# Optimization experiments

Hardware: AMD Instinct MI355X
Metric: run time of the kernel (lower is better)

The kernel has to match this reference:

```python
import jax, jax.numpy as jnp
import numpy as np

T = 1024          # tokens (batch*seq, vLLM flattened layout)
D = 2048          # hidden_size
H = 16            # attention heads
HD = D // H       # head_dim = 128
E = 16            # num routed experts
K = 2             # top_k
IM = 1408         # moe_intermediate_size
IS = 5632         # shared_expert_intermediate_size
EPS = 1e-6
THETA = 10000.0


def setup_inputs() -> dict:
    key = jax.random.key(0)
    ks = jax.random.split(key, 14)
    s = 0.02  # weight scale
    n = jax.random.normal
    return {
        "positions": jnp.arange(T, dtype=jnp.int32),
        "hidden_states": n(ks[0], (T, D), jnp.float32),
        "ln1_w": 1.0 + s * n(ks[1], (D,), jnp.float32),
        "ln2_w": 1.0 + s * n(ks[2], (D,), jnp.float32),
        "qkv_w": s * n(ks[3], (D, 3 * H * HD), jnp.float32),
        "qkv_b": s * n(ks[4], (3 * H * HD,), jnp.float32),
        "o_w": s * n(ks[5], (H * HD, D), jnp.float32),
        "router_w": s * n(ks[6], (D, E), jnp.float32),
        "w_gate": s * n(ks[7], (E, D, IM), jnp.float32),
        "w_up": s * n(ks[8], (E, D, IM), jnp.float32),
        "w_down": s * n(ks[9], (E, IM, D), jnp.float32),
        "sh_gate_up": s * n(ks[10], (D, 2 * IS), jnp.float32),
        "sh_down": s * n(ks[11], (IS, D), jnp.float32),
        "sh_expert_gate": s * n(ks[12], (D, 1), jnp.float32),
    }


def _rmsnorm(x, w):
    var = jnp.mean(x * x, axis=-1, keepdims=True)
    return x * jax.lax.rsqrt(var + EPS) * w


def _rope(x, positions):
    # neox-style rotary: x [T, H, HD]
    half = HD // 2
    inv_freq = 1.0 / (THETA ** (jnp.arange(0, half, dtype=jnp.float32) / half * 1.0))
    inv_freq = 1.0 / (THETA ** (jnp.arange(0, HD, 2, dtype=jnp.float32) / HD))
    ang = positions.astype(jnp.float32)[:, None] * inv_freq  # [T, HD/2]
    cos = jnp.cos(ang)[:, None, :]
    sin = jnp.sin(ang)[:, None, :]
    x1, x2 = x[..., :half], x[..., half:]
    return jnp.concatenate([x1 * cos - x2 * sin, x2 * cos + x1 * sin], axis=-1)


def reference(positions, hidden_states, ln1_w, ln2_w, qkv_w, qkv_b, o_w,
              router_w, w_gate, w_up, w_down, sh_gate_up, sh_down,
              sh_expert_gate):
    # --- input RMSNorm (residual=None path) ---
    residual = hidden_states
    x = _rmsnorm(hidden_states, ln1_w)

    # --- self-attention: QKV + RoPE + causal SDPA + o_proj ---
    qkv = x @ qkv_w + qkv_b
    q, k, v = jnp.split(qkv, [H * HD, 2 * H * HD], axis=-1)
    q = _rope(q.reshape(T, H, HD), positions)
    k = _rope(k.reshape(T, H, HD), positions)
    v = v.reshape(T, H, HD)
    scale = HD ** -0.5
    scores = jnp.einsum('thd,shd->hts', q, k) * scale  # [H, T, T]
    causal = jnp.tril(jnp.ones((T, T), dtype=bool))
    scores = jnp.where(causal[None], scores, jnp.finfo(scores.dtype).min)
    attn = jax.nn.softmax(scores, axis=-1)
    ctx = jnp.einsum('hts,shd->thd', attn, v).reshape(T, H * HD)
    attn_out = ctx @ o_w

    # --- fused add + post-attention RMSNorm ---
    residual = residual + attn_out
    x = _rmsnorm(residual, ln2_w)

    # --- sparse MoE: router -> softmax -> top-k (renormalized) -> experts ---
    logits = x @ router_w                                    # [T, E]
    probs = jax.nn.softmax(logits.astype(jnp.float32), axis=-1)
    topv, topi = jax.lax.top_k(probs, K)                     # [T, K]
    topv = topv / jnp.sum(topv, axis=-1, keepdims=True)      # norm_topk_prob
    w = jnp.zeros((T, E), dtype=x.dtype).at[
        jnp.arange(T)[:, None], topi].set(topv.astype(x.dtype))
    g = jax.nn.silu(jnp.einsum('td,edi->tei', x, w_gate)) * \
        jnp.einsum('td,edi->tei', x, w_up)                   # [T, E, IM]
    moe_out = jnp.einsum('tei,eid,te->td', g, w_down, w)

    # --- shared expert with sigmoid gate ---
    gu = x @ sh_gate_up
    g2, u2 = jnp.split(gu, 2, axis=-1)
    shared = (jax.nn.silu(g2) * u2) @ sh_down
    shared = jax.nn.sigmoid(x @ sh_expert_gate) * shared

    hidden_states = moe_out + shared
    return hidden_states, residual
```

## Files before the change

kernel.cpp:

```cpp
#include <hip/hip_runtime.h>

constexpr int T_  = 1024;
constexpr int D_  = 2048;
constexpr int H_  = 16;
constexpr int HD_ = 128;
constexpr int E_  = 16;
constexpr int IM_ = 1408;
constexpr int IS_ = 5632;

typedef __attribute__((ext_vector_type(8))) short bf16x8;
typedef __attribute__((ext_vector_type(4))) short short4v;
typedef __attribute__((ext_vector_type(4))) float f32x4;

__device__ __forceinline__ short f2bf(float f){
  unsigned u = __builtin_bit_cast(unsigned, f);
  u += 0x7fffu + ((u >> 16) & 1u);
  return (short)(u >> 16);
}
__device__ __forceinline__ float bf2f(short s){
  unsigned u = ((unsigned)(unsigned short)s) << 16;
  return __builtin_bit_cast(float, u);
}
__device__ __forceinline__ unsigned cvtpk(float lo, float hi){
  unsigned r;
  asm("v_cvt_pk_bf16_f32 %0, %1, %2" : "=v"(r) : "v"(lo), "v"(hi));
  return r;
}
__device__ __forceinline__ float pk_lo(unsigned h){
  return __builtin_bit_cast(float, h << 16);
}
__device__ __forceinline__ float pk_hi(unsigned h){
  return __builtin_bit_cast(float, h & 0xffff0000u);
}
__device__ __forceinline__ f32x4 mfma16(bf16x8 a, bf16x8 b, f32x4 c){
  return __builtin_amdgcn_mfma_f32_16x16x32_bf16(a, b, c, 0, 0, 0);
}
__device__ __forceinline__ void split3(float f, short& h, short& m, short& l){
  h = f2bf(f); float r = f - bf2f(h);
  m = f2bf(r); l = f2bf(r - bf2f(m));
}
__device__ __forceinline__ void split2(float f, short& h, short& m){
  h = f2bf(f); m = f2bf(f - bf2f(h));
}
__device__ __forceinline__ uint4 mk4(unsigned a, unsigned b, unsigned c, unsigned d){
  uint4 r; r.x=a; r.y=b; r.z=c; r.w=d; return r;
}

__global__ __launch_bounds__(256) void sctab_kernel(
    const int* __restrict__ pos, float* __restrict__ cst, float* __restrict__ snt)
{
  int idx = blockIdx.x * 256 + threadIdx.x;
  if (idx >= T_ * 64) return;
  int t = idx >> 6, i = idx & 63;
  float invf = (float)pow(10000.0, -(double)i / 64.0);
  float ang  = (float)pos[t] * invf;
  double s, c;
  sincos((double)ang, &s, &c);
  cst[idx] = (float)c; snt[idx] = (float)s;
}

__global__ __launch_bounds__(256) void rms_kernel(
    const float* __restrict__ x, const float* __restrict__ w,
    short* __restrict__ o0, short* __restrict__ o1, short* __restrict__ o2,
    short* __restrict__ ob, float* __restrict__ of)
{
  int t = blockIdx.x, tid = threadIdx.x;
  const float* xr = x + (size_t)t * D_;
  float4 va = ((const float4*)xr)[tid*2];
  float4 vb = ((const float4*)xr)[tid*2+1];
  float ss = va.x*va.x + va.y*va.y + va.z*va.z + va.w*va.w
           + vb.x*vb.x + vb.y*vb.y + vb.z*vb.z + vb.w*vb.w;
  for (int o = 32; o; o >>= 1) ss += __shfl_xor(ss, o, 64);
  __shared__ float red[4];
  int lane = tid & 63, wid = tid >> 6;
  if (lane == 0) red[wid] = ss;
  __syncthreads();
  ss = red[0] + red[1] + red[2] + red[3];
  float rs = 1.0f / sqrtf(ss * (1.0f/D_) + 1e-6f);
  float4 wa = ((const float4*)w)[tid*2];
  float4 wb = ((const float4*)w)[tid*2+1];
  float xv[8] = {va.x,va.y,va.z,va.w, vb.x,vb.y,vb.z,vb.w};
  float wv[8] = {wa.x,wa.y,wa.z,wa.w, wb.x,wb.y,wb.z,wb.w};
  size_t base = (size_t)t * D_ + tid*8;
  #pragma unroll
  for (int p = 0; p < 4; ++p){
    float f0 = xv[2*p]   * rs * wv[2*p];
    float f1 = xv[2*p+1] * rs * wv[2*p+1];
    if (o0){
      unsigned h = cvtpk(f0, f1);
      float r0 = f0 - pk_lo(h), r1 = f1 - pk_hi(h);
      unsigned m = cvtpk(r0, r1);
      unsigned l = cvtpk(r0 - pk_lo(m), r1 - pk_hi(m));
      *(unsigned*)&o0[base + 2*p] = h;
      *(unsigned*)&o1[base + 2*p] = m;
      *(unsigned*)&o2[base + 2*p] = l;
    }
    if (ob) *(unsigned*)&ob[base + 2*p] = cvtpk(f0, f1);
    if (of){ of[base + 2*p] = f0; of[base + 2*p + 1] = f1; }
  }
}

__global__ __launch_bounds__(256) void prepk_kernel(
    const float* __restrict__ qkv, const float* __restrict__ cst,
    const float* __restrict__ snt, short* __restrict__ Kp0, short* __restrict__ Kp1)
{
  int idx = blockIdx.x * 256 + threadIdx.x;
  int c = idx & 7, t = (idx >> 3) & (T_-1), h = idx >> 13;
  int d0 = c * 8;
  const float* kp = qkv + (size_t)t * (3*D_) + D_ + h*HD_;
  const float* cp = cst + t*64 + d0;
  const float* sp = snt + t*64 + d0;
  unsigned lh[4], ll[4], hh[4], hl[4];
  #pragma unroll
  for (int p = 0; p < 4; ++p){
    float xl0 = kp[d0+2*p],    xh0 = kp[d0+64+2*p];
    float xl1 = kp[d0+2*p+1],  xh1 = kp[d0+64+2*p+1];
    float cv0 = cp[2*p], sv0 = sp[2*p], cv1 = cp[2*p+1], sv1 = sp[2*p+1];
    float rl0 = xl0*cv0 - xh0*sv0, rh0 = xh0*cv0 + xl0*sv0;
    float rl1 = xl1*cv1 - xh1*sv1, rh1 = xh1*cv1 + xl1*sv1;
    unsigned a = cvtpk(rl0, rl1);
    ll[p] = cvtpk(rl0 - pk_lo(a), rl1 - pk_hi(a)); lh[p] = a;
    unsigned b = cvtpk(rh0, rh1);
    hl[p] = cvtpk(rh0 - pk_lo(b), rh1 - pk_hi(b)); hh[p] = b;
  }
  size_t ob = ((size_t)h*T_ + t) * HD_;
  *(uint4*)(Kp0 + ob + d0)      = mk4(lh[0],lh[1],lh[2],lh[3]);
  *(uint4*)(Kp0 + ob + 64 + d0) = mk4(hh[0],hh[1],hh[2],hh[3]);
  *(uint4*)(Kp1 + ob + d0)      = mk4(ll[0],ll[1],ll[2],ll[3]);
  *(uint4*)(Kp1 + ob + 64 + d0) = mk4(hl[0],hl[1],hl[2],hl[3]);
}

__global__ __launch_bounds__(256) void prepv_kernel(
    const float* __restrict__ qkv, short* __restrict__ Vp0, short* __restrict__ Vp1)
{
  __shared__ short Vl[2][128][72];
  int t0 = blockIdx.x * 64, h = blockIdx.y, tid = threadIdx.x;
  int r = tid >> 2, cq = (tid & 3) * 32;
  const float* src = qkv + (size_t)(t0+r) * (3*D_) + 2*D_ + h*HD_ + cq;
  #pragma unroll
  for (int jj = 0; jj < 8; ++jj){
    float4 v = *(const float4*)(src + jj*4);
    float vv[4] = {v.x, v.y, v.z, v.w};
    #pragma unroll
    for (int u = 0; u < 4; ++u){
      int d = cq + jj*4 + u;
      short a, b; split2(vv[u], a, b);
      Vl[0][d][r] = a; Vl[1][d][r] = b;
    }
  }
  __syncthreads();
  int d = tid >> 1, tc = (tid & 1) * 32;
  short* dst0 = Vp0 + ((size_t)h*HD_ + d) * T_ + t0 + tc;
  short* dst1 = Vp1 + ((size_t)h*HD_ + d) * T_ + t0 + tc;
  #pragma unroll
  for (int q = 0; q < 4; ++q){
    *(uint4*)(dst0 + q*8) = *(const uint4*)&Vl[0][d][tc + q*8];
    *(uint4*)(dst1 + q*8) = *(const uint4*)&Vl[1][d][tc + q*8];
  }
}

__global__ __launch_bounds__(256) void prepw_kernel(
    const float* __restrict__ w, short* __restrict__ P0, short* __restrict__ P1)
{
  __shared__ short L0[64][72], L1[64][72];
  int k0 = blockIdx.x * 64, n0 = blockIdx.y * 64;
  int tid = threadIdx.x;
  int r = tid >> 2, cq = (tid & 3) * 16;
  const float* src = w + (size_t)(k0 + r) * D_ + n0 + cq;
  #pragma unroll
  for (int q = 0; q < 4; ++q){
    float4 f = *(const float4*)(src + q*4);
    float fv[4] = {f.x, f.y, f.z, f.w};
    #pragma unroll
    for (int u = 0; u < 4; ++u){
      int n = cq + q*4 + u;
      short a, b; split2(fv[u], a, b);
      L0[n][r] = a; L1[n][r] = b;
    }
  }
  __syncthreads();
  int n = tid >> 2, kq = (tid & 3) * 16;
  short* d0 = P0 + (size_t)(n0 + n) * D_ + k0 + kq;
  short* d1 = P1 + (size_t)(n0 + n) * D_ + k0 + kq;
  *(uint4*)(d0)     = *(const uint4*)&L0[n][kq];
  *(uint4*)(d0 + 8) = *(const uint4*)&L0[n][kq + 8];
  *(uint4*)(d1)     = *(const uint4*)&L1[n][kq];
  *(uint4*)(d1 + 8) = *(const uint4*)&L1[n][kq + 8];
}

__global__ __launch_bounds__(128) void attn_kernel(
    const float* __restrict__ qkv,
    const float* __restrict__ cst, const float* __restrict__ snt,
    const short* __restrict__ Kp0, const short* __restrict__ Kp1,
    const short* __restrict__ Vp0, const short* __restrict__ Vp1,
    short* __restrict__ c0p, short* __restrict__ c1p, short* __restrict__ c2p)
{
  __shared__ __attribute__((aligned(16))) short Ks[2][2][32][128];
  __shared__ __attribute__((aligned(16))) short Vs[2][2][128][40];
  __shared__ __attribute__((aligned(16))) short Ps[3][2][16][40];

  const float SCALE = 0.08838834764831845f;
  const int QW = 3*D_;
  int h = blockIdx.x;
  int ys = blockIdx.y;
  int qt = (ys < 16) ? (ys*2) : ((31-ys)*2 + 1);
  int q0 = qt * 32;
  int tid = threadIdx.x, lane = tid & 63, wq = tid >> 6;
  int lr = lane & 15, kq8 = (lane >> 4) * 8, r4 = (lane >> 4) * 4;

  bf16x8 qfh[4], qfm[4], qfl[4];
  { int qrow = q0 + wq*16 + lr;
    const float* qp = qkv + (size_t)qrow * QW + h*HD_;
    const float* cp = cst + qrow*64;
    const float* sp = snt + qrow*64;
    float x[4][8], cs[2][8], sn[2][8], rot[4][8];
    for (int ks = 0; ks < 4; ++ks)
      for (int j = 0; j < 8; ++j) x[ks][j] = qp[ks*32 + kq8 + j];
    for (int hf = 0; hf < 2; ++hf)
      for (int j = 0; j < 8; ++j){
        cs[hf][j] = cp[hf*32 + kq8 + j];
        sn[hf][j] = sp[hf*32 + kq8 + j];
      }
    for (int j = 0; j < 8; ++j){
      rot[0][j] = x[0][j]*cs[0][j] - x[2][j]*sn[0][j];
      rot[1][j] = x[1][j]*cs[1][j] - x[3][j]*sn[1][j];
      rot[2][j] = x[2][j]*cs[0][j] + x[0][j]*sn[0][j];
      rot[3][j] = x[3][j]*cs[1][j] + x[1][j]*sn[1][j];
    }
    for (int ks = 0; ks < 4; ++ks)
      for (int j = 0; j < 8; ++j){
        short a, b, c; split3(rot[ks][j], a, b, c);
        qfh[ks][j] = a; qfm[ks][j] = b; qfl[ks][j] = c;
      }
  }

  f32x4 acc[8];
  for (int i = 0; i < 8; ++i) acc[i] = f32x4{0.f,0.f,0.f,0.f};
  float mrun[4] = {-1e30f,-1e30f,-1e30f,-1e30f};
  float lrun[4] = {0.f,0.f,0.f,0.f};

  int krow = tid >> 2, kc = (tid & 3) * 32;
  const short* kb0 = Kp0 + ((size_t)h*T_ + krow) * HD_ + kc;
  const short* kb1 = Kp1 + ((size_t)h*T_ + krow) * HD_ + kc;
  const short* vb0 = Vp0 + ((size_t)h*HD_ + tid) * T_;
  const short* vb1 = Vp1 + ((size_t)h*HD_ + tid) * T_;
  int xr = (krow & 7) * 8;

  uint4 kr0[4], kr1[4], vr0[4], vr1[4];
  auto LOAD = [&](int it){
    size_t ko = (size_t)it * 32 * HD_;
    const uint4* p0 = (const uint4*)(kb0 + ko);
    const uint4* p1 = (const uint4*)(kb1 + ko);
    #pragma unroll
    for (int g = 0; g < 4; ++g){ kr0[g] = p0[g]; kr1[g] = p1[g]; }
    const uint4* q0p = (const uint4*)(vb0 + it*32);
    const uint4* q1p = (const uint4*)(vb1 + it*32);
    #pragma unroll
    for (int g = 0; g < 4; ++g){ vr0[g] = q0p[g]; vr1[g] = q1p[g]; }
  };
  auto STORE = [&](int buf){
    #pragma unroll
    for (int g = 0; g < 4; ++g){
      int col = (kc + 8*g) ^ xr;
      *(uint4*)&Ks[buf][0][krow][col] = kr0[g];
      *(uint4*)&Ks[buf][1][krow][col] = kr1[g];
    }
    #pragma unroll
    for (int g = 0; g < 4; ++g){
      *(uint4*)&Vs[buf][0][tid][g*8] = vr0[g];
      *(uint4*)&Vs[buf][1][tid][g*8] = vr1[g];
    }
  };

  int nt = qt + 1;
  LOAD(0); STORE(0);
  if (nt > 1) LOAD(1);
  asm volatile("s_waitcnt lgkmcnt(0)" ::: "memory");
  __builtin_amdgcn_s_barrier();

  int cur = 0;
  for (int it = 0; it < nt; ++it){
    if (it + 1 < nt){
      STORE(cur ^ 1);
      if (it + 2 < nt) LOAD(it + 2);
    }
    int kv0 = it * 32;
    int xl = (lr & 7) * 8;
    f32x4 s0 = f32x4{0.f,0.f,0.f,0.f}, s1 = f32x4{0.f,0.f,0.f,0.f};
    #pragma unroll
    for (int ks = 0; ks < 4; ++ks){
      int col = (ks*32 + kq8) ^ xl;
      bf16x8 b0h = *(const bf16x8*)&Ks[cur][0][lr][col];
      bf16x8 b0m = *(const bf16x8*)&Ks[cur][1][lr][col];
      bf16x8 b1h = *(const bf16x8*)&Ks[cur][0][16+lr][col];
      bf16x8 b1m = *(const bf16x8*)&Ks[cur][1][16+lr][col];
      s0 = mfma16(qfh[ks], b0h, s0); s0 = mfma16(qfh[ks], b0m, s0);
      s0 = mfma16(qfm[ks], b0h, s0); s0 = mfma16(qfm[ks], b0m, s0);
      s0 = mfma16(qfl[ks], b0h, s0);
      s1 = mfma16(qfh[ks], b1h, s1); s1 = mfma16(qfh[ks], b1m, s1);
      s1 = mfma16(qfm[ks], b1h, s1); s1 = mfma16(qfm[ks], b1m, s1);
      s1 = mfma16(qfl[ks], b1h, s1);
    }
    float pm[2][4]; float alpha[4];
    for (int r = 0; r < 4; ++r){
      int qr = q0 + wq*16 + r4 + r;
      float x0 = s0[r]*SCALE, x1 = s1[r]*SCALE;
      if (kv0 + lr > qr)      x0 = -1e30f;
      if (kv0 + 16 + lr > qr) x1 = -1e30f;
      float mt_ = fmaxf(x0, x1);
      mt_ = fmaxf(mt_, __shfl_xor(mt_, 1, 64));
      mt_ = fmaxf(mt_, __shfl_xor(mt_, 2, 64));
      mt_ = fmaxf(mt_, __shfl_xor(mt_, 4, 64));
      mt_ = fmaxf(mt_, __shfl_xor(mt_, 8, 64));
      float mn = fmaxf(mrun[r], mt_);
      float p0 = __expf(x0 - mn), p1 = __expf(x1 - mn);
      pm[0][r] = p0; pm[1][r] = p1;
      float ls = p0 + p1;
      ls += __shfl_xor(ls, 1, 64); ls += __shfl_xor(ls, 2, 64);
      ls += __shfl_xor(ls, 4, 64); ls += __shfl_xor(ls, 8, 64);
      alpha[r] = __expf(mrun[r] - mn);
      lrun[r] = lrun[r]*alpha[r] + ls;
      mrun[r] = mn;
    }
    for (int dt = 0; dt < 8; ++dt){
      f32x4 a = acc[dt];
      a[0]*=alpha[0]; a[1]*=alpha[1]; a[2]*=alpha[2]; a[3]*=alpha[3];
      acc[dt] = a;
    }
    for (int nn = 0; nn < 2; ++nn)
      for (int r = 0; r < 4; ++r){
        short a, b, c; split3(pm[nn][r], a, b, c);
        Ps[0][wq][r4+r][nn*16+lr] = a;
        Ps[1][wq][r4+r][nn*16+lr] = b;
        Ps[2][wq][r4+r][nn*16+lr] = c;
      }
    bf16x8 pah = *(const bf16x8*)&Ps[0][wq][lr][kq8];
    bf16x8 pam = *(const bf16x8*)&Ps[1][wq][lr][kq8];
    bf16x8 pal = *(const bf16x8*)&Ps[2][wq][lr][kq8];
    #pragma unroll
    for (int dt = 0; dt < 8; ++dt){
      bf16x8 vbh = *(const bf16x8*)&Vs[cur][0][dt*16+lr][kq8];
      bf16x8 vbm = *(const bf16x8*)&Vs[cur][1][dt*16+lr][kq8];
      acc[dt] = mfma16(pah, vbh, acc[dt]);
      acc[dt] = mfma16(pah, vbm, acc[dt]);
      acc[dt] = mfma16(pam, vbh, acc[dt]);
      acc[dt] = mfma16(pam, vbm, acc[dt]);
      acc[dt] = mfma16(pal, vbh, acc[dt]);
    }
    asm volatile("s_waitcnt lgkmcnt(0)" ::: "memory");
    __builtin_amdgcn_s_barrier();
    cur ^= 1;
  }
  for (int dt = 0; dt < 8; ++dt)
    for (int r = 0; r < 4; ++r){
      int qr = q0 + wq*16 + r4 + r;
      float o = acc[dt][r] / lrun[r];
      size_t ix = (size_t)qr * D_ + h*HD_ + dt*16 + lr;
      short a, b, c; split3(o, a, b, c);
      c0p[ix] = a; c1p[ix] = b; c2p[ix] = c;
    }
}

enum { M_QKV = 0, M_OPROJ = 1 };

template<int MODE>
__global__ __launch_bounds__(256) void gemm3_kernel(
    const short* __restrict__ A0, const short* __restrict__ A1, const short* __restrict__ A2,
    const float* __restrict__ Bw,
    const short* __restrict__ Bp0, const short* __restrict__ Bp1,
    const float* __restrict__ bias, const float* __restrict__ addsrc,
    float* __restrict__ outF,
    int K, int lda, int ldb, int ldo)
{
  __shared__ __attribute__((aligned(16))) short As[2][3][64][40];
  __shared__ __attribute__((aligned(16))) short Bs[2][2][64][40];

  int m0 = blockIdx.y * 64, n0 = blockIdx.x * 64;
  int tid = threadIdx.x, lane = tid & 63, wid = tid >> 6;
  int wm = wid >> 1, wn = wid & 1;
  int lr = lane & 15, kq8 = (lane >> 4) * 8;

  f32x4 acc[2][2];
  for (int i = 0; i < 2; ++i)
    for (int j = 0; j < 2; ++j) acc[i][j] = f32x4{0.f,0.f,0.f,0.f};

  int arow = tid >> 2, ac = (tid & 3) * 8;
  const short* aP0 = A0 + (size_t)(m0 + arow) * lda + ac;
  const short* aP1 = A1 + (size_t)(m0 + arow) * lda + ac;
  const short* aP2 = A2 + (size_t)(m0 + arow) * lda + ac;
  int bn = tid & 63, bk0 = (tid >> 6) * 8;
  const float* bP  = Bw  ? (Bw + n0 + bn) : nullptr;
  const short* bq0 = Bp0 ? (Bp0 + (size_t)(n0 + bn) * K) : nullptr;
  const short* bq1 = Bp1 ? (Bp1 + (size_t)(n0 + bn) * K) : nullptr;

  uint4 ar0, ar1, ar2;
  float br[8];
  uint4 pb0, pb1;

  auto LOAD = [&](int kt){
    ar0 = *(const uint4*)(aP0 + kt*32);
    ar1 = *(const uint4*)(aP1 + kt*32);
    ar2 = *(const uint4*)(aP2 + kt*32);
    if constexpr (MODE == M_QKV){
      const float* p = bP + (size_t)(kt*32 + bk0) * ldb;
      #pragma unroll
      for (int j = 0; j < 8; ++j) br[j] = p[(size_t)j * ldb];
    } else {
      pb0 = *(const uint4*)(bq0 + kt*32 + bk0);
      pb1 = *(const uint4*)(bq1 + kt*32 + bk0);
    }
  };
  auto STORE = [&](int buf){
    *(uint4*)&As[buf][0][arow][ac] = ar0;
    *(uint4*)&As[buf][1][arow][ac] = ar1;
    *(uint4*)&As[buf][2][arow][ac] = ar2;
    if constexpr (MODE == M_QKV){
      unsigned hh[4], mm[4];
      #pragma unroll
      for (int p = 0; p < 4; ++p){
        float f0 = br[2*p], f1 = br[2*p+1];
        unsigned h = cvtpk(f0, f1);
        mm[p] = cvtpk(f0 - pk_lo(h), f1 - pk_hi(h));
        hh[p] = h;
      }
      *(uint4*)&Bs[buf][0][bn][bk0] = mk4(hh[0],hh[1],hh[2],hh[3]);
      *(uint4*)&Bs[buf][1][bn][bk0] = mk4(mm[0],mm[1],mm[2],mm[3]);
    } else {
      *(uint4*)&Bs[buf][0][bn][bk0] = pb0;
      *(uint4*)&Bs[buf][1][bn][bk0] = pb1;
    }
  };

  int NK = K / 32;
  LOAD(0); STORE(0);
  if (NK > 1) LOAD(1);
  asm volatile("s_waitcnt lgkmcnt(0)" ::: "memory");
  __builtin_amdgcn_s_barrier();

  int cur = 0;
  for (int kt = 0; kt < NK; ++kt){
    if (kt + 1 < NK){
      STORE(cur ^ 1);
      if (kt + 2 < NK) LOAD(kt + 2);
    }
    bf16x8 aH[2], aM[2], aL[2];
    #pragma unroll
    for (int mt = 0; mt < 2; ++mt){
      aH[mt] = *(const bf16x8*)&As[cur][0][wm*32 + mt*16 + lr][kq8];
      aM[mt] = *(const bf16x8*)&As[cur][1][wm*32 + mt*16 + lr][kq8];
      aL[mt] = *(const bf16x8*)&As[cur][2][wm*32 + mt*16 + lr][kq8];
    }
    #pragma unroll
    for (int nt = 0; nt < 2; ++nt){
      bf16x8 bH = *(const bf16x8*)&Bs[cur][0][wn*32 + nt*16 + lr][kq8];
      bf16x8 bM = *(const bf16x8*)&Bs[cur][1][wn*32 + nt*16 + lr][kq8];
      #pragma unroll
      for (int mt = 0; mt < 2; ++mt){
        f32x4 a = acc[mt][nt];
        a = mfma16(aH[mt], bH, a);
        a = mfma16(aH[mt], bM, a);
        a = mfma16(aM[mt], bH, a);
        a = mfma16(aM[mt], bM, a);
        a = mfma16(aL[mt], bH, a);
        acc[mt][nt] = a;
      }
    }
    asm volatile("s_waitcnt lgkmcnt(0)" ::: "memory");
    __builtin_amdgcn_s_barrier();
    cur ^= 1;
  }

  for (int mt = 0; mt < 2; ++mt)
    for (int nt = 0; nt < 2; ++nt)
      for (int r = 0; r < 4; ++r){
        int mrow = m0 + wm*32 + mt*16 + (lane >> 4)*4 + r;
        int col  = n0 + wn*32 + nt*16 + lr;
        float v = acc[mt][nt][r];
        if constexpr (MODE == M_QKV){
          outF[(size_t)mrow * ldo + col] = v + bias[col];
        } else {
          outF[(size_t)mrow * ldo + col] = v + addsrc[(size_t)mrow * ldo + col];
        }
      }
}

__global__ __launch_bounds__(256) void gu_kernel(
    const short* __restrict__ x2b,
    const float* __restrict__ w_gate, const float* __restrict__ w_up,
    const float* __restrict__ sh_gu,
    short* __restrict__ gbuf, short* __restrict__ sbuf,
    const int* __restrict__ perm, const int* __restrict__ offE,
    const int* __restrict__ cntE)
{
  __shared__ __attribute__((aligned(16))) short As[2][128][40];
  __shared__ __attribute__((aligned(16))) short Bs[2][2][64][40];

  int z = blockIdx.z;
  bool SH = (z == E_);
  int N    = SH ? IS_ : IM_;
  int n0 = blockIdx.x * 64;
  if (n0 >= N) return;
  int mcnt  = SH ? T_ : cntE[z];
  int mbase = SH ? 0  : offE[z];
  int m0 = blockIdx.y * 128;
  if (m0 >= mcnt) return;
  int ldb = SH ? 2*IS_ : IM_;
  int ldo = SH ? IS_   : IM_;
  const float* Bg = SH ? sh_gu        : (w_gate + (size_t)z * D_ * IM_);
  const float* Bu = SH ? (sh_gu + IS_) : (w_up  + (size_t)z * D_ * IM_);
  short* outB = SH ? sbuf : gbuf;

  int tid = threadIdx.x, lane = tid & 63, wid = tid >> 6;
  int wm = wid >> 1, wn = wid & 1;
  int lr = lane & 15, kq8 = (lane >> 4) * 8;

  f32x4 acc0[4][2], acc1[4][2];
  #pragma unroll
  for (int i = 0; i < 4; ++i)
    for (int j = 0; j < 2; ++j){
      acc0[i][j] = f32x4{0.f,0.f,0.f,0.f};
      acc1[i][j] = f32x4{0.f,0.f,0.f,0.f};
    }

  int arow = tid >> 1, acol = (tid & 1) * 16;
  int aRowIdx;
  { int mr = m0 + arow;
    int mc = (mr < mcnt) ? mr : 0;
    aRowIdx = SH ? mc : perm[mbase + mc];
  }
  const short* aP = x2b + (size_t)aRowIdx * D_;

  int bn_ = tid & 63, bkq = (tid >> 6) * 8;
  const float* bP0 = Bg + n0 + bn_;
  const float* bP1 = Bu + n0 + bn_;

  uint4 arA, arB;
  float br0[8], br1[8];

  auto LOAD = [&](int kt){
    const uint4* s = (const uint4*)(aP + kt*32 + acol);
    arA = s[0]; arB = s[1];
    const float* p0 = bP0 + (size_t)(kt*32 + bkq) * ldb;
    const float* p1 = bP1 + (size_t)(kt*32 + bkq) * ldb;
    #pragma unroll
    for (int j = 0; j < 8; ++j){ br0[j] = p0[(size_t)j * ldb]; br1[j] = p1[(size_t)j * ldb]; }
  };
  auto STORE = [&](int buf){
    *(uint4*)&As[buf][arow][acol]   = arA;
    *(uint4*)&As[buf][arow][acol+8] = arB;
    unsigned v0[4], v1[4];
    #pragma unroll
    for (int p = 0; p < 4; ++p){
      v0[p] = cvtpk(br0[2*p], br0[2*p+1]);
      v1[p] = cvtpk(br1[2*p], br1[2*p+1]);
    }
    *(uint4*)&Bs[buf][0][bn_][bkq] = mk4(v0[0],v0[1],v0[2],v0[3]);
    *(uint4*)&Bs[buf][1][bn_][bkq] = mk4(v1[0],v1[1],v1[2],v1[3]);
  };

  constexpr int NK = D_ / 32;
  LOAD(0); STORE(0);
  LOAD(1);
  asm volatile("s_waitcnt lgkmcnt(0)" ::: "memory");
  __builtin_amdgcn_s_barrier();

  int cur = 0;
  for (int kt = 0; kt < NK; ++kt){
    if (kt + 1 < NK){
      STORE(cur ^ 1);
      if (kt + 2 < NK) LOAD(kt + 2);
    }
    bf16x8 a[4];
    #pragma unroll
    for (int mt = 0; mt < 4; ++mt)
      a[mt] = *(const bf16x8*)&As[cur][wm*64 + mt*16 + lr][kq8];
    #pragma unroll
    for (int nt = 0; nt < 2; ++nt){
      int nrow = wn*32 + nt*16 + lr;
      bf16x8 b0 = *(const bf16x8*)&Bs[cur][0][nrow][kq8];
      bf16x8 b1 = *(const bf16x8*)&Bs[cur][1][nrow][kq8];
      #pragma unroll
      for (int mt = 0; mt < 4; ++mt){
        acc0[mt][nt] = mfma16(a[mt], b0, acc0[mt][nt]);
        acc1[mt][nt] = mfma16(a[mt], b1, acc1[mt][nt]);
      }
    }
    asm volatile("s_waitcnt lgkmcnt(0)" ::: "memory");
    __builtin_amdgcn_s_barrier();
    cur ^= 1;
  }

  for (int mt = 0; mt < 4; ++mt)
    for (int nt = 0; nt < 2; ++nt)
      for (int r = 0; r < 4; ++r){
        int mrow = m0 + wm*64 + mt*16 + (lane >> 4)*4 + r;
        if (mrow >= mcnt) continue;
        int col = n0 + wn*32 + nt*16 + lr;
        float v = acc0[mt][nt][r];
        float u = acc1[mt][nt][r];
        float sv = v / (1.f + __expf(-v)) * u;
        outB[(size_t)(mbase + mrow) * ldo + col] = f2bf(sv);
      }
}

__global__ __launch_bounds__(256) void dn_kernel(
    const short* __restrict__ gbuf, const short* __restrict__ sbuf,
    const float* __restrict__ w_down, const float* __restrict__ sh_down,
    float* __restrict__ outF,
    const int* __restrict__ perm, const int* __restrict__ offE,
    const int* __restrict__ cntE, const float* __restrict__ wgt,
    const float* __restrict__ sig)
{
  __shared__ __attribute__((aligned(16))) short As[2][128][40];
  __shared__ __attribute__((aligned(16))) short Bs[2][64][40];

  int z = blockIdx.z;
  bool SH = (z == E_);
  int K = SH ? IS_ : IM_;
  int mcnt  = SH ? T_ : cntE[z];
  int mbase = SH ? 0  : offE[z];
  int m0 = blockIdx.y * 128;
  if (m0 >= mcnt) return;
  int n0 = blockIdx.x * 64;
  const float* Bq = SH ? sh_down : (w_down + (size_t)z * IM_ * D_);
  const short* Ab = SH ? sbuf : gbuf;

  int tid = threadIdx.x, lane = tid & 63, wid = tid >> 6;
  int wm = wid >> 1, wn = wid & 1;
  int lr = lane & 15, kq8 = (lane >> 4) * 8;

  f32x4 acc0[4][2];
  #pragma unroll
  for (int i = 0; i < 4; ++i)
    for (int j = 0; j < 2; ++j) acc0[i][j] = f32x4{0.f,0.f,0.f,0.f};

  int arow = tid >> 1, acol = (tid & 1) * 16;
  int mr = m0 + arow;
  int mc = (mr < mcnt) ? mr : 0;
  const short* aP = Ab + (size_t)(SH ? mc : (mbase + mc)) * K;

  int bn_ = tid & 63, bkq = (tid >> 6) * 8;
  const float* bP0 = Bq + n0 + bn_;

  uint4 arA, arB;
  float br0[8];

  auto LOAD = [&](int kt){
    const uint4* s = (const uint4*)(aP + kt*32 + acol);
    arA = s[0]; arB = s[1];
    const float* p0 = bP0 + (size_t)(kt*32 + bkq) * D_;
    #pragma unroll
    for (int j = 0; j < 8; ++j) br0[j] = p0[(size_t)j * D_];
  };
  auto STORE = [&](int buf){
    *(uint4*)&As[buf][arow][acol]   = arA;
    *(uint4*)&As[buf][arow][acol+8] = arB;
    unsigned v0[4];
    #pragma unroll
    for (int p = 0; p < 4; ++p) v0[p] = cvtpk(br0[2*p], br0[2*p+1]);
    *(uint4*)&Bs[buf][bn_][bkq] = mk4(v0[0],v0[1],v0[2],v0[3]);
  };

  int NK = K / 32;
  LOAD(0); STORE(0);
  LOAD(1);
  asm volatile("s_waitcnt lgkmcnt(0)" ::: "memory");
  __builtin_amdgcn_s_barrier();

  int cur = 0;
  for (int kt = 0; kt < NK; ++kt){
    if (kt + 1 < NK){
      STORE(cur ^ 1);
      if (kt + 2 < NK) LOAD(kt + 2);
    }
    bf16x8 a[4];
    #pragma unroll
    for (int mt = 0; mt < 4; ++mt)
      a[mt] = *(const bf16x8*)&As[cur][wm*64 + mt*16 + lr][kq8];
    #pragma unroll
    for (int nt = 0; nt < 2; ++nt){
      bf16x8 b0 = *(const bf16x8*)&Bs[cur][wn*32 + nt*16 + lr][kq8];
      #pragma unroll
      for (int mt = 0; mt < 4; ++mt)
        acc0[mt][nt] = mfma16(a[mt], b0, acc0[mt][nt]);
    }
    asm volatile("s_waitcnt lgkmcnt(0)" ::: "memory");
    __builtin_amdgcn_s_barrier();
    cur ^= 1;
  }

  for (int mt = 0; mt < 4; ++mt)
    for (int nt = 0; nt < 2; ++nt)
      for (int r = 0; r < 4; ++r){
        int mrow = m0 + wm*64 + mt*16 + (lane >> 4)*4 + r;
        if (mrow >= mcnt) continue;
        int col = n0 + wn*32 + nt*16 + lr;
        float v = acc0[mt][nt][r];
        if (SH){
          atomicAdd(&outF[(size_t)mrow * D_ + col], sig[mrow] * v);
        } else {
          int tk = perm[mbase + mrow];
          atomicAdd(&outF[(size_t)tk * D_ + col], v * wgt[mbase + mrow]);
        }
      }
}

__global__ __launch_bounds__(256) void router_kernel(
    const float* __restrict__ x2f, const float* __restrict__ rw,
    const float* __restrict__ seg, int* __restrict__ te, float* __restrict__ tw,
    float* __restrict__ sig, int* __restrict__ cnt)
{
  int t = blockIdx.x, tid = threadIdx.x, lane = tid & 63, w = tid >> 6;
  const float* xr = x2f + (size_t)t * D_;
  float a0 = 0.f, a1 = 0.f, a2 = 0.f, a3 = 0.f, ag = 0.f;
  for (int j = 0; j < 32; ++j){
    int d = lane + 64*j;
    float xv = xr[d];
    const float* rp = rw + (size_t)d * E_ + w*4;
    a0 += xv * rp[0]; a1 += xv * rp[1]; a2 += xv * rp[2]; a3 += xv * rp[3];
    ag += xv * seg[d];
  }
  for (int o = 32; o; o >>= 1){
    a0 += __shfl_xor(a0, o, 64); a1 += __shfl_xor(a1, o, 64);
    a2 += __shfl_xor(a2, o, 64); a3 += __shfl_xor(a3, o, 64);
    ag += __shfl_xor(ag, o, 64);
  }
  __shared__ float lg[16];
  __shared__ float sgv;
  if (lane == 0){
    lg[w*4+0] = a0; lg[w*4+1] = a1; lg[w*4+2] = a2; lg[w*4+3] = a3;
    if (w == 0) sgv = ag;
  }
  __syncthreads();
  if (tid == 0){
    int e0 = 0; float v0 = lg[0];
    for (int ee = 1; ee < 16; ++ee) if (lg[ee] > v0){ v0 = lg[ee]; e0 = ee; }
    int e1 = -1; float v1 = -3e38f;
    for (int ee = 0; ee < 16; ++ee){
      if (ee == e0) continue;
      if (lg[ee] > v1){ v1 = lg[ee]; e1 = ee; }
    }
    float w0 = 1.f / (1.f + expf(v1 - v0));
    te[2*t] = e0; te[2*t+1] = e1;
    tw[2*t] = w0; tw[2*t+1] = 1.f - w0;
    atomicAdd(&cnt[e0], 1); atomicAdd(&cnt[e1], 1);
    sig[t] = 1.f / (1.f + expf(-sgv));
  }
}

__global__ void prefix_kernel(const int* __restrict__ cnt, int* __restrict__ offE,
                              int* __restrict__ cursor)
{
  if (threadIdx.x == 0){
    int s = 0;
    for (int e = 0; e < 16; ++e){ offE[e] = s; s += cnt[e]; }
  }
  if (threadIdx.x < 16) cursor[threadIdx.x] = 0;
}

__global__ __launch_bounds__(256) void scatter_kernel(
    const int* __restrict__ te, const float* __restrict__ tw,
    const int* __restrict__ offE, int* __restrict__ cursor,
    int* __restrict__ perm, float* __restrict__ wgt)
{
  int t = blockIdx.x * 256 + threadIdx.x;
  if (t >= T_) return;
  for (int i = 0; i < 2; ++i){
    int e = te[2*t + i];
    int pos = offE[e] + atomicAdd(&cursor[e], 1);
    perm[pos] = t; wgt[pos] = tw[2*t + i];
  }
}

extern "C" void kernel_launch(void* const* d_in, const int* in_sizes, int n_in,
                              void* d_out, int out_size, void* d_ws, size_t ws_size,
                              hipStream_t stream)
{
  const int*   positions = (const int*)  d_in[0];
  const float* hidden    = (const float*)d_in[1];
  const float* ln1       = (const float*)d_in[2];
  const float* ln2       = (const float*)d_in[3];
  const float* qkv_w     = (const float*)d_in[4];
  const float* qkv_b     = (const float*)d_in[5];
  const float* o_w       = (const float*)d_in[6];
  const float* router_w  = (const float*)d_in[7];
  const float* w_gate    = (const float*)d_in[8];
  const float* w_up      = (const float*)d_in[9];
  const float* w_down    = (const float*)d_in[10];
  const float* sh_gu     = (const float*)d_in[11];
  const float* sh_down   = (const float*)d_in[12];
  const float* sh_eg     = (const float*)d_in[13];

  float* out_hidden = (float*)d_out;
  float* out_resid  = (float*)d_out + (size_t)T_ * D_;

  char* wp = (char*)d_ws;
  auto alloc = [&](size_t b){ char* p = wp; wp += (b + 255) & ~(size_t)255; return p; };

  float* qkv  = (float*)alloc((size_t)T_ * 3*D_ * 4);
  short* x1h  = (short*)alloc((size_t)T_ * D_ * 2);
  short* x1m  = (short*)alloc((size_t)T_ * D_ * 2);
  short* x1l  = (short*)alloc((size_t)T_ * D_ * 2);
  short* Kp0  = (short*)alloc((size_t)T_ * D_ * 2);
  short* Kp1  = (short*)alloc((size_t)T_ * D_ * 2);
  short* Vp0  = (short*)alloc((size_t)T_ * D_ * 2);
  short* Vp1  = (short*)alloc((size_t)T_ * D_ * 2);
  float* cst  = (float*)alloc((size_t)T_ * 64 * 4);
  float* snt  = (float*)alloc((size_t)T_ * 64 * 4);
  int*   te   = (int*)  alloc(2*T_*4);
  float* tw   = (float*)alloc(2*T_*4);
  float* sig  = (float*)alloc(T_*4);
  int*   cnt    = (int*)alloc(256);
  int*   offE   = (int*)alloc(256);
  int*   cursor = (int*)alloc(256);
  int*   perm = (int*)  alloc(2*T_*4);
  float* wgt  = (float*)alloc(2*T_*4);

  short* ctxh = x1h;
  short* ctxm = x1m;
  short* ctxl = x1l;
  float* x2f  = qkv;
  short* sbuf = (short*)((char*)qkv + (size_t)8388608);
  short* gbuf = (short*)x1h;
  short* x2b  = (short*)((char*)x1h + (size_t)5767168);
  short* Wo0  = Kp0;
  short* Wo1  = Vp0;

  hipMemsetAsync(cnt, 0, 64, stream);
  hipMemsetAsync(out_hidden, 0, (size_t)T_ * D_ * 4, stream);

  sctab_kernel<<<(T_*64)/256, 256, 0, stream>>>(positions, cst, snt);

  rms_kernel<<<T_, 256, 0, stream>>>(hidden, ln1, x1h, x1m, x1l, nullptr, nullptr);

  gemm3_kernel<M_QKV><<<dim3(96, 16), 256, 0, stream>>>(
      x1h, x1m, x1l, qkv_w, nullptr, nullptr, qkv_b, nullptr, qkv,
      D_, D_, 3*D_, 3*D_);

  prepk_kernel<<<(T_*H_*8)/256, 256, 0, stream>>>(qkv, cst, snt, Kp0, Kp1);
  prepv_kernel<<<dim3(16, 16), 256, 0, stream>>>(qkv, Vp0, Vp1);

  attn_kernel<<<dim3(16, 32), 128, 0, stream>>>(
      qkv, cst, snt, Kp0, Kp1, Vp0, Vp1, ctxh, ctxm, ctxl);

  prepw_kernel<<<dim3(32, 32), 256, 0, stream>>>(o_w, Wo0, Wo1);

  gemm3_kernel<M_OPROJ><<<dim3(32, 16), 256, 0, stream>>>(
      ctxh, ctxm, ctxl, nullptr, Wo0, Wo1, nullptr, hidden, out_resid,
      D_, D_, D_, D_);

  rms_kernel<<<T_, 256, 0, stream>>>(out_resid, ln2, nullptr, nullptr, nullptr, x2b, x2f);

  router_kernel<<<T_, 256, 0, stream>>>(x2f, router_w, sh_eg, te, tw, sig, cnt);
  prefix_kernel<<<1, 64, 0, stream>>>(cnt, offE, cursor);
  scatter_kernel<<<4, 256, 0, stream>>>(te, tw, offE, cursor, perm, wgt);

  gu_kernel<<<dim3(88, 8, 17), 256, 0, stream>>>(
      x2b, w_gate, w_up, sh_gu, gbuf, sbuf, perm, offE, cnt);

  dn_kernel<<<dim3(32, 8, 17), 256, 0, stream>>>(
      gbuf, sbuf, w_down, sh_down, out_hidden, perm, offE, cnt, wgt, sig);

  (void)in_sizes; (void)n_in; (void)out_size; (void)ws_size;
}
```

Measured before the change: 876.3 us.

## Deepen GEMM global-load prefetch to two tiles ahead with dual register sets

The three GEMM kernels (gemm3, gate/up, down) now keep two register staging sets and unroll the k-loop by two. Global loads for tile kt+2 or kt+3 are issued while earlier tiles are stored to LDS and computed, so each load has more time in flight before it is consumed. The trade-off is higher register pressure, which could lower occupancy. Odd-NK handling relies on guards, and the gate/up and down loops assume an even NK.

```diff
diff --git a/kernel.cpp b/kernel.cpp
--- a/kernel.cpp
+++ b/kernel.cpp
@@ -45,6 +45,8 @@
 __device__ __forceinline__ uint4 mk4(unsigned a, unsigned b, unsigned c, unsigned d){
   uint4 r; r.x=a; r.y=b; r.z=c; r.w=d; return r;
 }
+#define LGKM0_BAR() do{ asm volatile("s_waitcnt lgkmcnt(0)" ::: "memory"); \
+                        __builtin_amdgcn_s_barrier(); }while(0)
 
 __global__ __launch_bounds__(256) void sctab_kernel(
     const int* __restrict__ pos, float* __restrict__ cst, float* __restrict__ snt)
@@ -275,8 +277,7 @@
   int nt = qt + 1;
   LOAD(0); STORE(0);
   if (nt > 1) LOAD(1);
-  asm volatile("s_waitcnt lgkmcnt(0)" ::: "memory");
-  __builtin_amdgcn_s_barrier();
+  LGKM0_BAR();
 
   int cur = 0;
   for (int it = 0; it < nt; ++it){
@@ -347,8 +348,7 @@
       acc[dt] = mfma16(pam, vbm, acc[dt]);
       acc[dt] = mfma16(pal, vbh, acc[dt]);
     }
-    asm volatile("s_waitcnt lgkmcnt(0)" ::: "memory");
-    __builtin_amdgcn_s_barrier();
+    LGKM0_BAR();
     cur ^= 1;
   }
   for (int dt = 0; dt < 8; ++dt)
@@ -393,56 +393,75 @@
   const short* bq0 = Bp0 ? (Bp0 + (size_t)(n0 + bn) * K) : nullptr;
   const short* bq1 = Bp1 ? (Bp1 + (size_t)(n0 + bn) * K) : nullptr;
 
-  uint4 ar0, ar1, ar2;
-  float br[8];
-  uint4 pb0, pb1;
-
-  auto LOAD = [&](int kt){
-    ar0 = *(const uint4*)(aP0 + kt*32);
-    ar1 = *(const uint4*)(aP1 + kt*32);
-    ar2 = *(const uint4*)(aP2 + kt*32);
+  uint4 ar0_0, ar1_0, ar2_0, ar0_1, ar1_1, ar2_1;
+  float br_0[8], br_1[8];
+  uint4 pb0_0, pb1_0, pb0_1, pb1_1;
+
+  auto LOAD0 = [&](int kt){
+    ar0_0 = *(const uint4*)(aP0 + kt*32);
+    ar1_0 = *(const uint4*)(aP1 + kt*32);
+    ar2_0 = *(const uint4*)(aP2 + kt*32);
     if constexpr (MODE == M_QKV){
       const float* p = bP + (size_t)(kt*32 + bk0) * ldb;
       #pragma unroll
-      for (int j = 0; j < 8; ++j) br[j] = p[(size_t)j * ldb];
+      for (int j = 0; j < 8; ++j) br_0[j] = p[(size_t)j * ldb];
     } else {
-      pb0 = *(const uint4*)(bq0 + kt*32 + bk0);
-      pb1 = *(const uint4*)(bq1 + kt*32 + bk0);
-    }
-  };
-  auto STORE = [&](int buf){
-    *(uint4*)&As[buf][0][arow][ac] = ar0;
-    *(uint4*)&As[buf][1][arow][ac] = ar1;
-    *(uint4*)&As[buf][2][arow][ac] = ar2;
+      pb0_0 = *(const uint4*)(bq0 + kt*32 + bk0);
+      pb1_0 = *(const uint4*)(bq1 + kt*32 + bk0);
+    }
+  };
+  auto LOAD1 = [&](int kt){
+    ar0_1 = *(const uint4*)(aP0 + kt*32);
+    ar1_1 = *(const uint4*)(aP1 + kt*32);
+    ar2_1 = *(const uint4*)(aP2 + kt*32);
+    if constexpr (MODE == M_QKV){
+      const float* p = bP + (size_t)(kt*32 + bk0) * ldb;
+      #pragma unroll
+      for (int j = 0; j < 8; ++j) br_1[j] = p[(size_t)j * ldb];
+    } else {
+      pb0_1 = *(const uint4*)(bq0 + kt*32 + bk0);
+      pb1_1 = *(const uint4*)(bq1 + kt*32 + bk0);
+    }
+  };
+  auto STORE0 = [&](int buf){
+    *(uint4*)&As[buf][0][arow][ac] = ar0_0;
+    *(uint4*)&As[buf][1][arow][ac] = ar1_0;
+    *(uint4*)&As[buf][2][arow][ac] = ar2_0;
     if constexpr (MODE == M_QKV){
       unsigned hh[4], mm[4];
       #pragma unroll
       for (int p = 0; p < 4; ++p){
-        float f0 = br[2*p], f1 = br[2*p+1];
-        unsigned h = cvtpk(f0, f1);
-        mm[p] = cvtpk(f0 - pk_lo(h), f1 - pk_hi(h));
+        unsigned h = cvtpk(br_0[2*p], br_0[2*p+1]);
+        mm[p] = cvtpk(br_0[2*p] - pk_lo(h), br_0[2*p+1] - pk_hi(h));
         hh[p] = h;
       }
       *(uint4*)&Bs[buf][0][bn][bk0] = mk4(hh[0],hh[1],hh[2],hh[3]);
       *(uint4*)&Bs[buf][1][bn][bk0] = mk4(mm[0],mm[1],mm[2],mm[3]);
     } else {
-      *(uint4*)&Bs[buf][0][bn][bk0] = pb0;
-      *(uint4*)&Bs[buf][1][bn][bk0] = pb1;
-    }
-  };
-
-  int NK = K / 32;
-  LOAD(0); STORE(0);
-  if (NK > 1) LOAD(1);
-  asm volatile("s_waitcnt lgkmcnt(0)" ::: "memory");
-  __builtin_amdgcn_s_barrier();
-
-  int cur = 0;
-  for (int kt = 0; kt < NK; ++kt){
-    if (kt + 1 < NK){
-      STORE(cur ^ 1);
-      if (kt + 2 < NK) LOAD(kt + 2);
-    }
+      *(uint4*)&Bs[buf][0][bn][bk0] = pb0_0;
+      *(uint4*)&Bs[buf][1][bn][bk0] = pb1_0;
+    }
+  };
+  auto STORE1 = [&](int buf){
+    *(uint4*)&As[buf][0][arow][ac] = ar0_1;
+    *(uint4*)&As[buf][1][arow][ac] = ar1_1;
+    *(uint4*)&As[buf][2][arow][ac] = ar2_1;
+    if constexpr (MODE == M_QKV){
+      unsigned hh[4], mm[4];
+      #pragma unroll
+      for (int p = 0; p < 4; ++p){
+        unsigned h = cvtpk(br_1[2*p], br_1[2*p+1]);
+        mm[p] = cvtpk(br_1[2*p] - pk_lo(h), br_1[2*p+1] - pk_hi(h));
+        hh[p] = h;
+      }
+      *(uint4*)&Bs[buf][0][bn][bk0] = mk4(hh[0],hh[1],hh[2],hh[3]);
+      *(uint4*)&Bs[buf][1][bn][bk0] = mk4(mm[0],mm[1],mm[2],mm[3]);
+    } else {
+      *(uint4*)&Bs[buf][0][bn][bk0] = pb0_1;
+      *(uint4*)&Bs[buf][1][bn][bk0] = pb1_1;
+    }
+  };
+  auto COMPUTE = [&](int cur){
     bf16x8 aH[2], aM[2], aL[2];
     #pragma unroll
     for (int mt = 0; mt < 2; ++mt){
@@ -465,9 +484,28 @@
         acc[mt][nt] = a;
       }
     }
-    asm volatile("s_waitcnt lgkmcnt(0)" ::: "memory");
-    __builtin_amdgcn_s_barrier();
+  };
+
+  int NK = K / 32;
+  LOAD0(0); LOAD1(1);
+  STORE0(0);
+  LOAD0(2);
+  LGKM0_BAR();
+
+  int cur = 0;
+  for (int kt = 0; kt < NK; kt += 2){
+    if (kt + 1 < NK) STORE1(cur ^ 1);
+    if (kt + 3 < NK) LOAD1(kt + 3);
+    COMPUTE(cur);
+    LGKM0_BAR();
     cur ^= 1;
+    if (kt + 1 < NK){
+      if (kt + 2 < NK) STORE0(cur ^ 1);
+      if (kt + 4 < NK) LOAD0(kt + 4);
+      COMPUTE(cur);
+      LGKM0_BAR();
+      cur ^= 1;
+    }
   }
 
   for (int mt = 0; mt < 2; ++mt)
@@ -506,8 +544,8 @@
   if (m0 >= mcnt) return;
   int ldb = SH ? 2*IS_ : IM_;
   int ldo = SH ? IS_   : IM_;
-  const float* Bg = SH ? sh_gu        : (w_gate + (size_t)z * D_ * IM_);
-  const float* Bu = SH ? (sh_gu + IS_) : (w_up  + (size_t)z * D_ * IM_);
+  const float* Bg = SH ? sh_gu         : (w_gate + (size_t)z * D_ * IM_);
+  const float* Bu = SH ? (sh_gu + IS_) : (w_up   + (size_t)z * D_ * IM_);
   short* outB = SH ? sbuf : gbuf;
 
   int tid = threadIdx.x, lane = tid & 63, wid = tid >> 6;
@@ -534,42 +572,50 @@
   const float* bP0 = Bg + n0 + bn_;
   const float* bP1 = Bu + n0 + bn_;
 
-  uint4 arA, arB;
-  float br0[8], br1[8];
-
-  auto LOAD = [&](int kt){
+  uint4 arA_0, arB_0, arA_1, arB_1;
+  float br0_0[8], br1_0[8], br0_1[8], br1_1[8];
+
+  auto LOAD0 = [&](int kt){
     const uint4* s = (const uint4*)(aP + kt*32 + acol);
-    arA = s[0]; arB = s[1];
+    arA_0 = s[0]; arB_0 = s[1];
     const float* p0 = bP0 + (size_t)(kt*32 + bkq) * ldb;
     const float* p1 = bP1 + (size_t)(kt*32 + bkq) * ldb;
     #pragma unroll
-    for (int j = 0; j < 8; ++j){ br0[j] = p0[(size_t)j * ldb]; br1[j] = p1[(size_t)j * ldb]; }
-  };
-  auto STORE = [&](int buf){
-    *(uint4*)&As[buf][arow][acol]   = arA;
-    *(uint4*)&As[buf][arow][acol+8] = arB;
+    for (int j = 0; j < 8; ++j){ br0_0[j] = p0[(size_t)j * ldb]; br1_0[j] = p1[(size_t)j * ldb]; }
+  };
+  auto LOAD1 = [&](int kt){
+    const uint4* s = (const uint4*)(aP + kt*32 + acol);
+    arA_1 = s[0]; arB_1 = s[1];
+    const float* p0 = bP0 + (size_t)(kt*32 + bkq) * ldb;
+    const float* p1 = bP1 + (size_t)(kt*32 + bkq) * ldb;
+    #pragma unroll
+    for (int j = 0; j < 8; ++j){ br0_1[j] = p0[(size_t)j * ldb]; br1_1[j] = p1[(size_t)j * ldb]; }
+  };
+  auto STORE0 = [&](int buf){
+    *(uint4*)&As[buf][arow][acol]   = arA_0;
+    *(uint4*)&As[buf][arow][acol+8] = arB_0;
     unsigned v0[4], v1[4];
     #pragma unroll
     for (int p = 0; p < 4; ++p){
-      v0[p] = cvtpk(br0[2*p], br0[2*p+1]);
-      v1[p] = cvtpk(br1[2*p], br1[2*p+1]);
+      v0[p] = cvtpk(br0_0[2*p], br0_0[2*p+1]);
+      v1[p] = cvtpk(br1_0[2*p], br1_0[2*p+1]);
     }
     *(uint4*)&Bs[buf][0][bn_][bkq] = mk4(v0[0],v0[1],v0[2],v0[3]);
     *(uint4*)&Bs[buf][1][bn_][bkq] = mk4(v1[0],v1[1],v1[2],v1[3]);
   };
-
-  constexpr int NK = D_ / 32;
-  LOAD(0); STORE(0);
-  LOAD(1);
-  asm volatile("s_waitcnt lgkmcnt(0)" ::: "memory");
-  __builtin_amdgcn_s_barrier();
-
-  int cur = 0;
-  for (int kt = 0; kt < NK; ++kt){
-    if (kt + 1 < NK){
-      STORE(cur ^ 1);
-      if (kt + 2 < NK) LOAD(kt + 2);
-    }
+  auto STORE1 = [&](int buf){
+    *(uint4*)&As[buf][arow][acol]   = arA_1;
+    *(uint4*)&As[buf][arow][acol+8] = arB_1;
+    unsigned v0[4], v1[4];
+    #pragma unroll
+    for (int p = 0; p < 4; ++p){
+      v0[p] = cvtpk(br0_1[2*p], br0_1[2*p+1]);
+      v1[p] = cvtpk(br1_1[2*p], br1_1[2*p+1]);
+    }
+    *(uint4*)&Bs[buf][0][bn_][bkq] = mk4(v0[0],v0[1],v0[2],v0[3]);
+    *(uint4*)&Bs[buf][1][bn_][bkq] = mk4(v1[0],v1[1],v1[2],v1[3]);
+  };
+  auto COMPUTE = [&](int cur){
     bf16x8 a[4];
     #pragma unroll
     for (int mt = 0; mt < 4; ++mt)
@@ -585,8 +631,25 @@
         acc1[mt][nt] = mfma16(a[mt], b1, acc1[mt][nt]);
       }
     }
-    asm volatile("s_waitcnt lgkmcnt(0)" ::: "memory");
-    __builtin_amdgcn_s_barrier();
+  };
+
+  constexpr int NK = D_ / 32;
+  LOAD0(0); LOAD1(1);
+  STORE0(0);
+  LOAD0(2);
+  LGKM0_BAR();
+
+  int cur = 0;
+  for (int kt = 0; kt < NK; kt += 2){
+    if (kt + 1 < NK) STORE1(cur ^ 1);
+    if (kt + 3 < NK) LOAD1(kt + 3);
+    COMPUTE(cur);
+    LGKM0_BAR();
+    cur ^= 1;
+    if (kt + 2 < NK) STORE0(cur ^ 1);
+    if (kt + 4 < NK) LOAD0(kt + 4);
+    COMPUTE(cur);
+    LGKM0_BAR();
     cur ^= 1;
   }
 
@@ -642,37 +705,40 @@
   int bn_ = tid & 63, bkq = (tid >> 6) * 8;
   const float* bP0 = Bq + n0 + bn_;
 
-  uint4 arA, arB;
-  float br0[8];
-
-  auto LOAD = [&](int kt){
+  uint4 arA_0, arB_0, arA_1, arB_1;
+  float br_0[8], br_1[8];
+
+  auto LOAD0 = [&](int kt){
     const uint4* s = (const uint4*)(aP + kt*32 + acol);
-    arA = s[0]; arB = s[1];
+    arA_0 = s[0]; arB_0 = s[1];
     const float* p0 = bP0 + (size_t)(kt*32 + bkq) * D_;
     #pragma unroll
-    for (int j = 0; j < 8; ++j) br0[j] = p0[(size_t)j * D_];
-  };
-  auto STORE = [&](int buf){
-    *(uint4*)&As[buf][arow][acol]   = arA;
-    *(uint4*)&As[buf][arow][acol+8] = arB;
+    for (int j = 0; j < 8; ++j) br_0[j] = p0[(size_t)j * D_];
+  };
+  auto LOAD1 = [&](int kt){
+    const uint4* s = (const uint4*)(aP + kt*32 + acol);
+    arA_1 = s[0]; arB_1 = s[1];
+    const float* p0 = bP0 + (size_t)(kt*32 + bkq) * D_;
+    #pragma unroll
+    for (int j = 0; j < 8; ++j) br_1[j] = p0[(size_t)j * D_];
+  };
+  auto STORE0 = [&](int buf){
+    *(uint4*)&As[buf][arow][acol]   = arA_0;
+    *(uint4*)&As[buf][arow][acol+8] = arB_0;
     unsigned v0[4];
     #pragma unroll
-    for (int p = 0; p < 4; ++p) v0[p] = cvtpk(br0[2*p], br0[2*p+1]);
+    for (int p = 0; p < 4; ++p) v0[p] = cvtpk(br_0[2*p], br_0[2*p+1]);
     *(uint4*)&Bs[buf][bn_][bkq] = mk4(v0[0],v0[1],v0[2],v0[3]);
   };
-
-  int NK = K / 32;
-  LOAD(0); STORE(0);
-  LOAD(1);
-  asm volatile("s_waitcnt lgkmcnt(0)" ::: "memory");
-  __builtin_amdgcn_s_barrier();
-
-  int cur = 0;
-  for (int kt = 0; kt < NK; ++kt){
-    if (kt + 1 < NK){
-      STORE(cur ^ 1);
-      if (kt + 2 < NK) LOAD(kt + 2);
-    }
+  auto STORE1 = [&](int buf){
+    *(uint4*)&As[buf][arow][acol]   = arA_1;
+    *(uint4*)&As[buf][arow][acol+8] = arB_1;
+    unsigned v0[4];
+    #pragma unroll
+    for (int p = 0; p < 4; ++p) v0[p] = cvtpk(br_1[2*p], br_1[2*p+1]);
+    *(uint4*)&Bs[buf][bn_][bkq] = mk4(v0[0],v0[1],v0[2],v0[3]);
+  };
+  auto COMPUTE = [&](int cur){
     bf16x8 a[4];
     #pragma unroll
     for (int mt = 0; mt < 4; ++mt)
@@ -684,8 +750,25 @@
       for (int mt = 0; mt < 4; ++mt)
         acc0[mt][nt] = mfma16(a[mt], b0, acc0[mt][nt]);
     }
-    asm volatile("s_waitcnt lgkmcnt(0)" ::: "memory");
-    __builtin_amdgcn_s_barrier();
+  };
+
+  int NK = K / 32;
+  LOAD0(0); LOAD1(1);
+  STORE0(0);
+  LOAD0(2);
+  LGKM0_BAR();
+
+  int cur = 0;
+  for (int kt = 0; kt < NK; kt += 2){
+    if (kt + 1 < NK) STORE1(cur ^ 1);
+    if (kt + 3 < NK) LOAD1(kt + 3);
+    COMPUTE(cur);
+    LGKM0_BAR();
+    cur ^= 1;
+    if (kt + 2 < NK) STORE0(cur ^ 1);
+    if (kt + 4 < NK) LOAD0(kt + 4);
+    COMPUTE(cur);
+    LGKM0_BAR();
     cur ^= 1;
   }
 
```

Measured after the change: 965.6 us. +10.2%, slower.
